# Optimization experiments

Measured on AMD Instinct MI355X. Metric: run time of the kernel, lower is better.

## Reference

```python
import jax, jax.numpy as jnp
import numpy as np
from jax import lax

IMG = 256   # model img_size
O = 7       # adaptive pool output size (out_size)
R = 32      # number of ROIs
B = 8       # batch
CF = 32     # UNet output channels
FOUT = 512  # fc out_features


def _conv(x, w, b):
    y = lax.conv_general_dilated(x, w, (1, 1), 'SAME',
                                 dimension_numbers=('NCHW', 'OIHW', 'NCHW'))
    return y + b[None, :, None, None]


def _pool(x):
    return lax.reduce_window(x, -jnp.inf, lax.max, (1, 1, 2, 2), (1, 1, 2, 2), 'VALID')


def _up(x):
    return jnp.repeat(jnp.repeat(x, 2, axis=2), 2, axis=3)


def _unet(x, p):
    r = jax.nn.relu
    e1 = r(_conv(r(_conv(x, p['e1w1'], p['e1b1'])), p['e1w2'], p['e1b2']))          # [B,32,H,W]
    e2 = r(_conv(r(_conv(_pool(e1), p['e2w1'], p['e2b1'])), p['e2w2'], p['e2b2']))  # [B,64,H/2,W/2]
    bo = r(_conv(r(_conv(_pool(e2), p['bw1'], p['bb1'])), p['bw2'], p['bb2']))      # [B,128,H/4,W/4]
    u2 = r(_conv(_up(bo), p['u2w'], p['u2b']))                                      # [B,64,H/2,W/2]
    d2 = r(_conv(r(_conv(jnp.concatenate([u2, e2], 1), p['d2w1'], p['d2b1'])), p['d2w2'], p['d2b2']))
    u1 = r(_conv(_up(d2), p['u1w'], p['u1b']))                                      # [B,32,H,W]
    d1 = r(_conv(r(_conv(jnp.concatenate([u1, e1], 1), p['d1w1'], p['d1b1'])), p['d1w2'], p['d1b2']))
    return _conv(d1, p['fw'], p['fb'])                                              # [B,CF,H,W]


def _adaptive_pool(ii, boxes):
    # Exact F.adaptive_avg_pool2d bins via an integral image.
    # ii: [B,C,H+1,W+1] (zero-padded 2D cumsum); boxes: [R,4] int (x1,y1,x2,y2).
    i = jnp.arange(O)
    h = boxes[:, 3] - boxes[:, 1]
    w = boxes[:, 2] - boxes[:, 0]
    sy = boxes[:, 1:2] + (i[None, :] * h[:, None]) // O            # floor(i*h/O)
    ey = boxes[:, 1:2] + ((i[None, :] + 1) * h[:, None] + O - 1) // O  # ceil((i+1)*h/O)
    sx = boxes[:, 0:1] + (i[None, :] * w[:, None]) // O
    ex = boxes[:, 0:1] + ((i[None, :] + 1) * w[:, None] + O - 1) // O
    yA, yB = sy[:, :, None], ey[:, :, None]   # [R,O,1]
    xA, xB = sx[:, None, :], ex[:, None, :]   # [R,1,O]
    s = ii[:, :, yB, xB] - ii[:, :, yA, xB] - ii[:, :, yB, xA] + ii[:, :, yA, xA]  # [B,C,R,O,O]
    area = ((ey - sy)[:, :, None] * (ex - sx)[:, None, :]).astype(ii.dtype)        # [R,O,O]
    return s / area[None, None]


def _forward(x, rois, p):
    H, W = x.shape[2], x.shape[3]
    xs, ys = IMG // H, IMG // W  # matches torch: x_scale, y_scale = img_size//m, img_size//n
    boxes = rois // jnp.array([xs, ys, xs, ys], dtype=rois.dtype)
    f = _unet(x, p)                                   # [B,CF,H,W]
    ii = jnp.pad(jnp.cumsum(jnp.cumsum(f, axis=2), axis=3),
                 ((0, 0), (0, 0), (1, 0), (1, 0)))    # integral image [B,CF,H+1,W+1]
    rp = _adaptive_pool(ii, boxes)                    # [B,CF,R,O,O]
    roi_feat = jnp.transpose(rp, (0, 2, 1, 3, 4)).reshape(x.shape[0], boxes.shape[0] * f.shape[1], O, O)
    gbox = jnp.array([[0, 0, W, H]], dtype=boxes.dtype)
    gpool = _adaptive_pool(ii, gbox)[:, :, 0]         # [B,CF,O,O]
    out = jnp.concatenate([gpool, roi_feat], axis=1)  # [B,(R+1)*CF,O,O]
    out = out.reshape(out.shape[0], out.shape[1], O * O)
    return jnp.einsum('bnk,fk->bnf', out, p['fcw']) + p['fcb']


_PNAMES = ['e1w1','e1b1','e1w2','e1b2','e2w1','e2b1','e2w2','e2b2','bw1','bb1','bw2','bb2',
           'u2w','u2b','d2w1','d2b1','d2w2','d2b2','u1w','u1b','d1w1','d1b1','d1w2','d1b2',
           'fw','fb','fcw','fcb']


def setup_inputs() -> dict:
    key = jax.random.key(0)
    ks = jax.random.split(key, 32)

    def w(k, shape):
        fan = int(np.prod(shape[1:]))
        return jax.random.normal(k, shape, jnp.float32) * np.sqrt(2.0 / fan)

    d = {}
    d['x'] = jax.random.normal(ks[0], (B, 3, IMG, IMG), jnp.float32)
    xy1 = jax.random.randint(ks[1], (R, 2), 0, 192)
    wh = jax.random.randint(ks[2], (R, 2), 16, 64)
    d['rois'] = jnp.concatenate([xy1, xy1 + wh], axis=1).astype(jnp.int32)  # (x1,y1,x2,y2)

    shapes = {'e1w1': (32, 3, 3, 3), 'e1w2': (32, 32, 3, 3),
              'e2w1': (64, 32, 3, 3), 'e2w2': (64, 64, 3, 3),
              'bw1': (128, 64, 3, 3), 'bw2': (128, 128, 3, 3),
              'u2w': (64, 128, 3, 3),
              'd2w1': (64, 128, 3, 3), 'd2w2': (64, 64, 3, 3),
              'u1w': (32, 64, 3, 3),
              'd1w1': (32, 64, 3, 3), 'd1w2': (32, 32, 3, 3),
              'fw': (CF, 32, 1, 1),
              'fcw': (FOUT, O * O)}
    i = 3
    for n, s in shapes.items():
        d[n] = w(ks[i], s); i += 1
        bn = n.replace('w', 'b', 1) if 'w' in n else n
        d[bn] = jnp.zeros((s[0],), jnp.float32)
    d['fcb'] = jnp.zeros((FOUT,), jnp.float32)
    return d


def reference(x, rois, e1w1, e1b1, e1w2, e1b2, e2w1, e2b1, e2w2, e2b2,
              bw1, bb1, bw2, bb2, u2w, u2b, d2w1, d2b1, d2w2, d2b2,
              u1w, u1b, d1w1, d1b1, d1w2, d1b2, fw, fb, fcw, fcb):
    p = dict(e1w1=e1w1, e1b1=e1b1, e1w2=e1w2, e1b2=e1b2, e2w1=e2w1, e2b1=e2b1,
             e2w2=e2w2, e2b2=e2b2, bw1=bw1, bb1=bb1, bw2=bw2, bb2=bb2,
             u2w=u2w, u2b=u2b, d2w1=d2w1, d2b1=d2b1, d2w2=d2w2, d2b2=d2b2,
             u1w=u1w, u1b=u1b, d1w1=d1w1, d1b1=d1b1, d1w2=d1w2, d1b2=d1b2,
             fw=fw, fb=fb, fcw=fcw, fcb=fcb)
    return _forward(x, rois, p)
```

## Files before the change

kernel.cpp:

```cpp
#include <hip/hip_runtime.h>

typedef _Float16 half8 __attribute__((ext_vector_type(8)));
typedef float f32x4 __attribute__((ext_vector_type(4)));
typedef float f32x16 __attribute__((ext_vector_type(16)));

__device__ __forceinline__ unsigned short f2h(float f) {
    _Float16 h = (_Float16)f;
    return __builtin_bit_cast(unsigned short, h);
}
__device__ __forceinline__ float h2f(unsigned short u) {
    return (float)__builtin_bit_cast(_Float16, u);
}

__device__ __forceinline__ void lds_load16(const uint4* g, uint4* l) {
    __builtin_amdgcn_global_load_lds(
        (const __attribute__((address_space(1))) unsigned int*)g,
        (__attribute__((address_space(3))) unsigned int*)l, 16, 0, 0);
}

#define IIROW 260
#define IIPLANE 66824

__global__ void wprep_k(const float* __restrict__ src, unsigned short* __restrict__ dst,
                        int Cout, int Cin, int total)
{
    int t = blockIdx.x * 256 + threadIdx.x;
    if (t >= total) return;
    int j = t & 7; int r = t >> 3;
    int co = r % Cout; r /= Cout;
    int oct = r & 3; r >>= 2;
    int pos = r % 9; int ck = r / 9;
    int ci = ck * 32 + oct * 8 + j;
    dst[t] = f2h(src[((size_t)co * Cin + ci) * 9 + pos]);
}

__global__ void w1prep_k(const float* __restrict__ src, unsigned short* __restrict__ dst)
{
    int t = blockIdx.x * 256 + threadIdx.x;
    if (t >= 4096) return;
    int j = t & 7, co = (t >> 3) & 31, koct = t >> 8;
    dst[t] = f2h(src[co * 32 + koct * 8 + j]);
}

__global__ void fct_k(const float* __restrict__ src, float* __restrict__ dst)
{
    int t = blockIdx.x * 256 + threadIdx.x;
    if (t >= 49 * 512) return;
    int k = t >> 9, f = t & 511;
    dst[t] = src[f * 49 + k];
}

template<int BM, int TW, int TH, int LW, int UP>
__global__ __launch_bounds__(256) void convm2_k(
    const uint4* __restrict__ in1, int C1g,
    const uint4* __restrict__ in2, int C2g,
    const uint4* __restrict__ wt,
    const float* __restrict__ bias,
    unsigned short* __restrict__ out,
    int Cout, int relu, const uint4* __restrict__ zp)
{
    constexpr int NM = BM / 16;
    constexpr int NN = (TW * TH) / 64;
    constexpr int Wf = 1 << LW, Hf = Wf;
    constexpr int WC = TW + 2, HR = TH + 2;
    constexpr int IN_GR = 4 * HR * WC;
    constexpr int LTW = (TW == 64) ? 6 : ((TW == 32) ? 5 : 7);
    constexpr int sH = UP ? (Hf >> 1) : Hf;
    constexpr int sW = UP ? (Wf >> 1) : Wf;
    __shared__ uint4 smem[IN_GR + 36 * BM];

    const int tid = threadIdx.x;
    const int lane = tid & 63, wv = tid >> 6;
    const int ng = Cout / BM;
    const int b = blockIdx.z / ng, cg = blockIdx.z % ng;
    const int x0 = blockIdx.x * TW, y0 = blockIdx.y * TH;
    const int NCK = (C1g + C2g) / 4;

    f32x4 acc[NM][NN];
#pragma unroll
    for (int m = 0; m < NM; ++m)
#pragma unroll
        for (int n = 0; n < NN; ++n) acc[m][n] = (f32x4){0.f, 0.f, 0.f, 0.f};

    const int l15 = lane & 15, l4 = lane >> 4;
    const int laneB = l4 * HR * WC + l15;
    const int laneA = l4 * BM + l15;

    for (int ck = 0; ck < NCK; ++ck) {
        if (ck) __syncthreads();
        {
            const uint4* src; int cg0, srcCg;
            if (ck * 4 < C1g) { src = in1; cg0 = ck * 4; srcCg = C1g; }
            else              { src = in2; cg0 = ck * 4 - C1g; srcCg = C2g; }
            for (int i = tid; i < IN_GR; i += 256) {
                int oct = i / (HR * WC);
                int rem = i - oct * (HR * WC);
                int row = rem / WC;
                int col = rem - row * WC;
                int gy = y0 + row - 1, gx = x0 + col - 1;
                int sy = UP ? (gy >> 1) : gy, sx = UP ? (gx >> 1) : gx;
                const uint4* ga = ((unsigned)gy < (unsigned)Hf && (unsigned)gx < (unsigned)Wf)
                    ? src + ((((size_t)b * sH + sy) * sW + sx) * srcCg + cg0 + oct)
                    : zp + (i & 63);
                lds_load16(ga, &smem[i]);
            }
        }
        {
            const uint4* wck = wt + (size_t)ck * 36 * Cout + (size_t)cg * BM;
            for (int i = tid; i < 36 * BM; i += 256) {
                int seg = i / BM, col = i - seg * BM;
                lds_load16(wck + seg * Cout + col, &smem[IN_GR + i]);
            }
        }
        __syncthreads();
        const half8* sB = (const half8*)smem;
        const half8* sA = (const half8*)(smem + IN_GR);
#pragma unroll
        for (int pos = 0; pos < 9; ++pos) {
            const int dr = pos / 3, dc = pos - dr * 3;
            half8 af[NM], bfr[NN];
#pragma unroll
            for (int m = 0; m < NM; ++m)
                af[m] = sA[pos * 4 * BM + m * 16 + laneA];
#pragma unroll
            for (int n = 0; n < NN; ++n) {
                const int pb = wv * (NN * 16) + n * 16;
                const int rn = (pb >> LTW) + dr;
                const int xn = (pb & (TW - 1)) + dc;
                bfr[n] = sB[rn * WC + xn + laneB];
            }
#pragma unroll
            for (int m = 0; m < NM; ++m)
#pragma unroll
                for (int n = 0; n < NN; ++n)
                    acc[m][n] = __builtin_amdgcn_mfma_f32_16x16x32_f16(af[m], bfr[n], acc[m][n], 0, 0, 0);
        }
    }

#pragma unroll
    for (int m = 0; m < NM; ++m) {
        const int co0 = cg * BM + m * 16 + l4 * 4;
        const float4 bs = *(const float4*)(bias + co0);
#pragma unroll
        for (int n = 0; n < NN; ++n) {
            const int pix = wv * (NN * 16) + n * 16 + l15;
            const int y = y0 + (pix >> LTW), x = x0 + (pix & (TW - 1));
            float v0 = acc[m][n][0] + bs.x;
            float v1 = acc[m][n][1] + bs.y;
            float v2 = acc[m][n][2] + bs.z;
            float v3 = acc[m][n][3] + bs.w;
            if (relu) {
                v0 = fmaxf(v0, 0.f); v1 = fmaxf(v1, 0.f);
                v2 = fmaxf(v2, 0.f); v3 = fmaxf(v3, 0.f);
            }
            uint2 pk;
            pk.x = (unsigned)f2h(v0) | ((unsigned)f2h(v1) << 16);
            pk.y = (unsigned)f2h(v2) | ((unsigned)f2h(v3) << 16);
            *(uint2*)(out + (((size_t)b * Hf + y) * Wf + x) * Cout + co0) = pk;
        }
    }
}

__global__ __launch_bounds__(256) void conv0_k(
    const float* __restrict__ in, const float* __restrict__ w,
    const float* __restrict__ bias, unsigned short* __restrict__ out)
{
    __shared__ float s_in[3][18][18];
    const int tx = threadIdx.x, ty = threadIdx.y;
    const int tid = ty * 16 + tx;
    const int b = blockIdx.z >> 2;
    const int coBase = (blockIdx.z & 3) * 8;
    const int bx = blockIdx.x * 16, by = blockIdx.y * 16;

    for (int i = tid; i < 3 * 18 * 18; i += 256) {
        int cc = i / 324, r = i % 324;
        int ly = r / 18, lx = r % 18;
        int gy = by + ly - 1, gx = bx + lx - 1;
        float v = 0.f;
        if ((unsigned)gy < 256u && (unsigned)gx < 256u)
            v = in[(((size_t)(b * 3 + cc)) << 16) + (gy << 8) + gx];
        ((float*)s_in)[i] = v;
    }
    __syncthreads();
    float acc[8];
#pragma unroll
    for (int k = 0; k < 8; ++k) acc[k] = 0.f;
    for (int cc = 0; cc < 3; ++cc) {
        float v[9];
#pragma unroll
        for (int dh = 0; dh < 3; ++dh)
#pragma unroll
            for (int dw = 0; dw < 3; ++dw)
                v[dh * 3 + dw] = s_in[cc][ty + dh][tx + dw];
        const float* wp = w + ((size_t)coBase * 3 + cc) * 9;
#pragma unroll
        for (int k = 0; k < 8; ++k) {
            const float* wk = wp + (size_t)k * 27;
            float a = acc[k];
#pragma unroll
            for (int j = 0; j < 9; ++j) a = fmaf(v[j], wk[j], a);
            acc[k] = a;
        }
    }
    const int h = by + ty, ww = bx + tx;
    unsigned short* op = out + (((size_t)(b * 256 + h)) * 256 + ww) * 32 + coBase;
#pragma unroll
    for (int k = 0; k < 8; ++k)
        op[k] = f2h(fmaxf(acc[k] + bias[coBase + k], 0.f));
}

__global__ void poolh_k(const uint4* __restrict__ in, uint4* __restrict__ out,
                        int Ho, int Wo, int C8, int total)
{
    int i = blockIdx.x * 256 + threadIdx.x;
    if (i >= total) return;
    int oct = i % C8; int p = i / C8;
    int x = p % Wo; p /= Wo;
    int y = p % Ho; int b = p / Ho;
    const int H = Ho * 2, W = Wo * 2;
    size_t g = (((size_t)b * H + 2 * y) * W + 2 * x) * C8 + oct;
    uint4 v00 = in[g], v01 = in[g + C8];
    uint4 v10 = in[g + (size_t)W * C8], v11 = in[g + (size_t)W * C8 + C8];
    const unsigned short* a0 = (const unsigned short*)&v00;
    const unsigned short* a1 = (const unsigned short*)&v01;
    const unsigned short* a2 = (const unsigned short*)&v10;
    const unsigned short* a3 = (const unsigned short*)&v11;
    uint4 res; unsigned short* rp = (unsigned short*)&res;
#pragma unroll
    for (int j = 0; j < 8; ++j)
        rp[j] = f2h(fmaxf(fmaxf(h2f(a0[j]), h2f(a1[j])), fmaxf(h2f(a2[j]), h2f(a3[j]))));
    out[(((size_t)b * Ho + y) * Wo + x) * C8 + oct] = res;
}

__global__ __launch_bounds__(256) void rowprep_k(
    const uint4* __restrict__ in, const uint4* __restrict__ w16,
    const float* __restrict__ bias, float* __restrict__ ii)
{
    __shared__ uint4 sIn[1024];
    __shared__ uint4 sW[128];
    __shared__ float sout[32][256];
    __shared__ float sb[32];
    const int tid = threadIdx.x;
    const int lane = tid & 63, wv = tid >> 6;
    const int l31 = lane & 31, l5 = lane >> 5;
    const int y = blockIdx.x, b = blockIdx.y;

    const uint4* ip = in + (((size_t)b * 256 + y) * 256) * 4;
#pragma unroll
    for (int it = 0; it < 4; ++it)
        lds_load16(ip + tid + it * 256, &sIn[tid + it * 256]);
    if (tid < 128) lds_load16(w16 + tid, &sW[tid]);
    if (tid < 32) sb[tid] = bias[tid];
    __syncthreads();

    const half8* hW = (const half8*)sW;
    const half8* hIn = (const half8*)sIn;
    half8 af0 = hW[l5 * 32 + l31];
    half8 af1 = hW[(2 + l5) * 32 + l31];
#pragma unroll
    for (int g = 0; g < 2; ++g) {
        const int p0 = wv * 64 + g * 32;
        half8 bf0 = hIn[(p0 + l31) * 4 + l5];
        half8 bf1 = hIn[(p0 + l31) * 4 + 2 + l5];
        f32x16 acc;
#pragma unroll
        for (int q = 0; q < 16; ++q) acc[q] = 0.f;
        acc = __builtin_amdgcn_mfma_f32_32x32x16_f16(af0, bf0, acc, 0, 0, 0);
        acc = __builtin_amdgcn_mfma_f32_32x32x16_f16(af1, bf1, acc, 0, 0, 0);
#pragma unroll
        for (int r = 0; r < 16; ++r) {
            const int co = (r & 3) + 8 * (r >> 2) + 4 * l5;
            sout[co][p0 + l31] = acc[r] + sb[co];
        }
    }
    __syncthreads();

    float* plane0 = ii + (size_t)(b * 32) * IIPLANE;
    if (y == 0) {
        for (int i = tid; i < 32 * 257; i += 256) {
            int c = i / 257, xx = i % 257;
            plane0[(size_t)c * IIPLANE + xx + 3] = 0.f;
        }
    }
    for (int cc = 0; cc < 8; ++cc) {
        const int c = wv * 8 + cc;
        float* prow = plane0 + (size_t)c * IIPLANE + (size_t)(y + 1) * IIROW;
        float4 v = *(const float4*)&sout[c][lane * 4];
        float s0 = v.x, s1 = s0 + v.y, s2 = s1 + v.z, s3 = s2 + v.w;
        float t = s3;
#pragma unroll
        for (int off = 1; off < 64; off <<= 1) {
            float u = __shfl_up(t, off);
            if (lane >= off) t += u;
        }
        const float base = t - s3;
        float4 o;
        o.x = base + s0; o.y = base + s1; o.z = base + s2; o.w = base + s3;
        *(float4*)(prow + 4 + lane * 4) = o;
        if (lane == 0) prow[3] = 0.f;
    }
}

__global__ __launch_bounds__(256) void colA_k(const float* __restrict__ ii,
                                              float* __restrict__ S)
{
    const int p = blockIdx.x, s = blockIdx.y;
    const int x = threadIdx.x;
    const float* plane = ii + (size_t)p * IIPLANE;
    float acc = 0.f;
#pragma unroll 8
    for (int y = s * 64 + 1; y <= s * 64 + 64; ++y)
        acc += plane[(size_t)y * IIROW + x + 4];
    S[(p * 3 + s) * 256 + x] = acc;
}

__global__ __launch_bounds__(256) void colB_k(float* __restrict__ ii,
                                              const float* __restrict__ S)
{
    const int p = blockIdx.x, s = blockIdx.y;
    const int x = threadIdx.x;
    float* plane = ii + (size_t)p * IIPLANE;
    float acc = 0.f;
    for (int t = 0; t < s; ++t) acc += S[(p * 3 + t) * 256 + x];
#pragma unroll 8
    for (int y = s * 64 + 1; y <= s * 64 + 64; ++y) {
        float* q = plane + (size_t)y * IIROW + x + 4;
        acc += *q;
        *q = acc;
    }
}

__global__ void pool_k(const float* __restrict__ ii, const int* __restrict__ rois,
                       float* __restrict__ pooled)
{
    int t = blockIdx.x * 256 + threadIdx.x;
    int k = t % 49; int nb = t / 49;
    int n = nb % 1056; int b = nb / 1056;
    int ki = k / 7, kj = k % 7;
    int x1, y1, x2, y2, c;
    if (n < 32) {
        x1 = 0; y1 = 0; x2 = 256; y2 = 256; c = n;
    } else {
        int r = (n - 32) >> 5;
        c = (n - 32) & 31;
        x1 = rois[r * 4 + 0]; y1 = rois[r * 4 + 1];
        x2 = rois[r * 4 + 2]; y2 = rois[r * 4 + 3];
    }
    const int h = y2 - y1, w = x2 - x1;
    const int sy = y1 + (ki * h) / 7, ey = y1 + ((ki + 1) * h + 6) / 7;
    const int sx = x1 + (kj * w) / 7, ex = x1 + ((kj + 1) * w + 6) / 7;
    const float* pl = ii + (size_t)(b * 32 + c) * IIPLANE + 3;
    float s = pl[ey * IIROW + ex] - pl[sy * IIROW + ex]
            - pl[ey * IIROW + sx] + pl[sy * IIROW + sx];
    pooled[t] = s / (float)((ey - sy) * (ex - sx));
}

__global__ __launch_bounds__(512) void fc_k(
    const float* __restrict__ pooled, const float* __restrict__ fcwT,
    const float* __restrict__ fcb, float* __restrict__ out)
{
    const int nt = blockIdx.x, b = blockIdx.y;
    const int f = threadIdx.x;
    float wr[49];
#pragma unroll
    for (int k = 0; k < 49; ++k) wr[k] = fcwT[k * 512 + f];
    const float base = fcb[f];
    const float* pr = pooled + ((size_t)b * 1056 + nt * 16) * 49;
    float* op = out + (((size_t)b * 1056 + nt * 16)) * 512 + f;
#pragma unroll
    for (int j = 0; j < 16; ++j) {
        float a = base;
#pragma unroll
        for (int k = 0; k < 49; ++k)
            a = fmaf(pr[j * 49 + k], wr[k], a);
        op[(size_t)j * 512] = a;
    }
}

extern "C" void kernel_launch(void* const* d_in, const int* in_sizes, int n_in,
                              void* d_out, int out_size, void* d_ws, size_t ws_size,
                              hipStream_t stream)
{
    const float* x    = (const float*)d_in[0];
    const int*   rois = (const int*)d_in[1];
    const float* e1w1 = (const float*)d_in[2];
    const float* e1b1 = (const float*)d_in[3];
    const float* e1w2 = (const float*)d_in[4];
    const float* e1b2 = (const float*)d_in[5];
    const float* e2w1 = (const float*)d_in[6];
    const float* e2b1 = (const float*)d_in[7];
    const float* e2w2 = (const float*)d_in[8];
    const float* e2b2 = (const float*)d_in[9];
    const float* bw1  = (const float*)d_in[10];
    const float* bb1  = (const float*)d_in[11];
    const float* bw2  = (const float*)d_in[12];
    const float* bb2  = (const float*)d_in[13];
    const float* u2w  = (const float*)d_in[14];
    const float* u2b  = (const float*)d_in[15];
    const float* d2w1 = (const float*)d_in[16];
    const float* d2b1 = (const float*)d_in[17];
    const float* d2w2 = (const float*)d_in[18];
    const float* d2b2 = (const float*)d_in[19];
    const float* u1w  = (const float*)d_in[20];
    const float* u1b  = (const float*)d_in[21];
    const float* d1w1 = (const float*)d_in[22];
    const float* d1b1 = (const float*)d_in[23];
    const float* d1w2 = (const float*)d_in[24];
    const float* d1b2 = (const float*)d_in[25];
    const float* fw   = (const float*)d_in[26];
    const float* fb   = (const float*)d_in[27];
    const float* fcw  = (const float*)d_in[28];
    const float* fcb  = (const float*)d_in[29];

    char* wsb = (char*)d_ws;
    char* WT = wsb;
    char* A  = wsb + 4194304;
    char* D  = A + 33554432;
    char* E  = D + 16777216;
    char* Bb = E + 16777216;
    char* C  = Bb + 33554432;
    char* F  = C + 8388608;
    float* ii     = (float*)F;
    float* fcwT   = (float*)(WT + 1179648);
    unsigned short* fw16 = (unsigned short*)(WT + 2097152);
    uint4* zp     = (uint4*)(WT + 4194304 - 8192);
    float* pooled = (float*)C;
    float* Sbuf   = (float*)(C + 2097152);
    hipMemsetAsync(zp, 0, 8192, stream);

    const float* wsrc[11] = {e1w2, e2w1, e2w2, bw1, bw2, u2w, d2w1, d2w2, u1w, d1w1, d1w2};
    const int wco[11] = {32, 64, 64, 128, 128, 64, 64, 64, 32, 32, 32};
    const int wci[11] = {32, 32, 64, 64, 128, 128, 128, 64, 64, 64, 32};
    size_t woff[11]; size_t o = 0;
    for (int i = 0; i < 11; ++i) { woff[i] = o; o += (size_t)wco[i] * wci[i] * 18; }
    for (int i = 0; i < 11; ++i) {
        int total = wco[i] * wci[i] * 9;
        hipLaunchKernelGGL(wprep_k, dim3((total + 255) / 256), dim3(256), 0, stream,
                           wsrc[i], (unsigned short*)(WT + woff[i]), wco[i], wci[i], total);
    }
    hipLaunchKernelGGL(fct_k, dim3((49 * 512 + 255) / 256), dim3(256), 0, stream, fcw, fcwT);
    hipLaunchKernelGGL(w1prep_k, dim3(16), dim3(256), 0, stream, fw, fw16);
    auto WP = [&](int i) { return (const uint4*)(WT + woff[i]); };

    #define CV1(i1,C1,i2,C2,wi,bs,ot,Cout,up,rl) \
        hipLaunchKernelGGL((convm2_k<32,64,4,8,up>), dim3(4,64,8*((Cout)/32)), dim3(256), 0, stream, \
            (const uint4*)(i1), (C1)/8, (const uint4*)(i2), (C2)/8, WP(wi), bs, \
            (unsigned short*)(ot), Cout, rl, zp)
    #define CV2(i1,C1,i2,C2,wi,bs,ot,Cout,up,rl) \
        hipLaunchKernelGGL((convm2_k<64,64,4,7,up>), dim3(2,32,8*((Cout)/64)), dim3(256), 0, stream, \
            (const uint4*)(i1), (C1)/8, (const uint4*)(i2), (C2)/8, WP(wi), bs, \
            (unsigned short*)(ot), Cout, rl, zp)
    #define CV3(i1,C1,i2,C2,wi,bs,ot,Cout,up,rl) \
        hipLaunchKernelGGL((convm2_k<32,64,4,6,up>), dim3(1,16,8*((Cout)/32)), dim3(256), 0, stream, \
            (const uint4*)(i1), (C1)/8, (const uint4*)(i2), (C2)/8, WP(wi), bs, \
            (unsigned short*)(ot), Cout, rl, zp)

    hipLaunchKernelGGL(conv0_k, dim3(16, 16, 32), dim3(16, 16), 0, stream,
                       x, e1w1, e1b1, (unsigned short*)A);
    CV1(A, 32, nullptr, 0, 0, e1b2, Bb, 32, 0, 1);
    {
        int N = 8 * 128 * 128 * 4;
        hipLaunchKernelGGL(poolh_k, dim3((N + 255) / 256), dim3(256), 0, stream,
                           (const uint4*)Bb, (uint4*)C, 128, 128, 4, N);
    }
    CV2(C, 32, nullptr, 0, 1, e2b1, A, 64, 0, 1);
    CV2(A, 64, nullptr, 0, 2, e2b2, D, 64, 0, 1);
    {
        int N = 8 * 64 * 64 * 8;
        hipLaunchKernelGGL(poolh_k, dim3((N + 255) / 256), dim3(256), 0, stream,
                           (const uint4*)D, (uint4*)C, 64, 64, 8, N);
    }
    CV3(C, 64, nullptr, 0, 3, bb1, E, 128, 0, 1);
    CV3(E, 128, nullptr, 0, 4, bb2, A, 128, 0, 1);
    CV2(A, 128, nullptr, 0, 5, u2b, E, 64, 1, 1);
    CV2(E, 64, D, 64, 6, d2b1, A, 64, 0, 1);
    CV2(A, 64, nullptr, 0, 7, d2b2, D, 64, 0, 1);
    CV1(D, 64, nullptr, 0, 8, u1b, A, 32, 1, 1);
    CV1(A, 32, Bb, 32, 9, d1b1, D, 32, 0, 1);
    CV1(D, 32, nullptr, 0, 10, d1b2, Bb, 32, 0, 1);
    hipLaunchKernelGGL(rowprep_k, dim3(256, 8), dim3(256), 0, stream,
                       (const uint4*)Bb, (const uint4*)fw16, fb, ii);
    hipLaunchKernelGGL(colA_k, dim3(256, 3), dim3(256), 0, stream, ii, Sbuf);
    hipLaunchKernelGGL(colB_k, dim3(256, 4), dim3(256), 0, stream, ii, Sbuf);
    hipLaunchKernelGGL(pool_k, dim3(8 * 1056 * 49 / 256), dim3(256), 0, stream,
                       ii, rois, pooled);
    hipLaunchKernelGGL(fc_k, dim3(66, 8), dim3(512), 0, stream,
                       pooled, fcwT, fcb, (float*)d_out);
    #undef CV1
    #undef CV2
    #undef CV3
}
```

Before: 400.7 us.

## Reuse input row fragments across kernel rows in MFMA conv with taller tiles

Restructures the conv inner loop so each wave loads RQ+2 input rows once per column offset and reuses them across the three kernel rows, instead of reloading B fragments for all nine taps. Tiles become 8 rows tall, with narrower widths for mid and low resolutions, and launch bounds request two blocks per CU. This cuts LDS reads per MFMA. In exchange, the larger input halo in LDS and the extra live fragments raise register and LDS pressure, and the grid has fewer blocks.

```diff
diff --git a/kernel.cpp b/kernel.cpp
--- a/kernel.cpp
+++ b/kernel.cpp
@@ -51,7 +51,7 @@
 }
 
 template<int BM, int TW, int TH, int LW, int UP>
-__global__ __launch_bounds__(256) void convm2_k(
+__global__ __launch_bounds__(256, 2) void convm4_k(
     const uint4* __restrict__ in1, int C1g,
     const uint4* __restrict__ in2, int C2g,
     const uint4* __restrict__ wt,
@@ -61,10 +61,13 @@
 {
     constexpr int NM = BM / 16;
     constexpr int NN = (TW * TH) / 64;
+    constexpr int CG = TW / 16;
+    constexpr int RQ = NN / CG;
+    static_assert(RQ == 2, "row-reuse layout needs 2 rows/wave");
     constexpr int Wf = 1 << LW, Hf = Wf;
     constexpr int WC = TW + 2, HR = TH + 2;
     constexpr int IN_GR = 4 * HR * WC;
-    constexpr int LTW = (TW == 64) ? 6 : ((TW == 32) ? 5 : 7);
+    constexpr int LTW = (TW == 64) ? 6 : 5;
     constexpr int sH = UP ? (Hf >> 1) : Hf;
     constexpr int sW = UP ? (Wf >> 1) : Wf;
     __shared__ uint4 smem[IN_GR + 36 * BM];
@@ -116,24 +119,28 @@
         const half8* sB = (const half8*)smem;
         const half8* sA = (const half8*)(smem + IN_GR);
 #pragma unroll
-        for (int pos = 0; pos < 9; ++pos) {
-            const int dr = pos / 3, dc = pos - dr * 3;
-            half8 af[NM], bfr[NN];
-#pragma unroll
-            for (int m = 0; m < NM; ++m)
-                af[m] = sA[pos * 4 * BM + m * 16 + laneA];
-#pragma unroll
-            for (int n = 0; n < NN; ++n) {
-                const int pb = wv * (NN * 16) + n * 16;
-                const int rn = (pb >> LTW) + dr;
-                const int xn = (pb & (TW - 1)) + dc;
-                bfr[n] = sB[rn * WC + xn + laneB];
+        for (int dc = 0; dc < 3; ++dc) {
+            half8 br[RQ + 2][CG];
+#pragma unroll
+            for (int r = 0; r < RQ + 2; ++r)
+#pragma unroll
+                for (int c2 = 0; c2 < CG; ++c2)
+                    br[r][c2] = sB[(wv * RQ + r) * WC + c2 * 16 + dc + laneB];
+#pragma unroll
+            for (int dr = 0; dr < 3; ++dr) {
+                half8 af[NM];
+#pragma unroll
+                for (int m = 0; m < NM; ++m)
+                    af[m] = sA[(dr * 3 + dc) * 4 * BM + m * 16 + laneA];
+#pragma unroll
+                for (int m = 0; m < NM; ++m)
+#pragma unroll
+                    for (int rq = 0; rq < RQ; ++rq)
+#pragma unroll
+                        for (int c2 = 0; c2 < CG; ++c2)
+                            acc[m][rq * CG + c2] = __builtin_amdgcn_mfma_f32_16x16x32_f16(
+                                af[m], br[rq + dr][c2], acc[m][rq * CG + c2], 0, 0, 0);
             }
-#pragma unroll
-            for (int m = 0; m < NM; ++m)
-#pragma unroll
-                for (int n = 0; n < NN; ++n)
-                    acc[m][n] = __builtin_amdgcn_mfma_f32_16x16x32_f16(af[m], bfr[n], acc[m][n], 0, 0, 0);
         }
     }
 
@@ -443,15 +450,15 @@
     auto WP = [&](int i) { return (const uint4*)(WT + woff[i]); };
 
     #define CV1(i1,C1,i2,C2,wi,bs,ot,Cout,up,rl) \
-        hipLaunchKernelGGL((convm2_k<32,64,4,8,up>), dim3(4,64,8*((Cout)/32)), dim3(256), 0, stream, \
+        hipLaunchKernelGGL((convm4_k<32,64,8,8,up>), dim3(4,32,8*((Cout)/32)), dim3(256), 0, stream, \
             (const uint4*)(i1), (C1)/8, (const uint4*)(i2), (C2)/8, WP(wi), bs, \
             (unsigned short*)(ot), Cout, rl, zp)
     #define CV2(i1,C1,i2,C2,wi,bs,ot,Cout,up,rl) \
-        hipLaunchKernelGGL((convm2_k<64,64,4,7,up>), dim3(2,32,8*((Cout)/64)), dim3(256), 0, stream, \
+        hipLaunchKernelGGL((convm4_k<64,32,8,7,up>), dim3(4,16,8*((Cout)/64)), dim3(256), 0, stream, \
             (const uint4*)(i1), (C1)/8, (const uint4*)(i2), (C2)/8, WP(wi), bs, \
             (unsigned short*)(ot), Cout, rl, zp)
     #define CV3(i1,C1,i2,C2,wi,bs,ot,Cout,up,rl) \
-        hipLaunchKernelGGL((convm2_k<32,64,4,6,up>), dim3(1,16,8*((Cout)/32)), dim3(256), 0, stream, \
+        hipLaunchKernelGGL((convm4_k<32,32,8,6,up>), dim3(2,8,8*((Cout)/32)), dim3(256), 0, stream, \
             (const uint4*)(i1), (C1)/8, (const uint4*)(i2), (C2)/8, WP(wi), bs, \
             (unsigned short*)(ot), Cout, rl, zp)
 
```

New measurement: 397.5 us. About the same (-0.8%).
